# Optimization experiments

Hardware: AMD Instinct MI355X
Metric: run time of the kernel (lower is better)

Reference implementation:

```python
import jax, jax.numpy as jnp
import numpy as np

P = 7            # cfg.POOLING_SIZE (= group_size)
N_CLASSES = 21   # PASCAL VOC incl. background
SPATIAL_SCALE = 1.0 / 16.0


def _round_half_up(x):
    # matches C round() for non-negative roi coords (jnp.round is banker's)
    return jnp.floor(x + 0.5)


def psroi_pool(feat, rois, out_dim):
    """Position-sensitive RoI average pooling via integral images.
    feat: [B, out_dim*P*P, H, W]; rois: [N, 5] (batch_idx, x1, y1, x2, y2).
    Returns [N, out_dim, P, P]."""
    B, C, H, W = feat.shape
    # summed-area table, zero-padded: S[b,c,h,w] = sum feat[b,c,:h,:w]
    S = jnp.cumsum(jnp.cumsum(feat, axis=2), axis=3)
    S = jnp.pad(S, ((0, 0), (0, 0), (1, 0), (1, 0)))

    b = rois[:, 0].astype(jnp.int32)
    x1 = _round_half_up(rois[:, 1]) * SPATIAL_SCALE
    y1 = _round_half_up(rois[:, 2]) * SPATIAL_SCALE
    x2 = _round_half_up(rois[:, 3] + 1.0) * SPATIAL_SCALE
    y2 = _round_half_up(rois[:, 4] + 1.0) * SPATIAL_SCALE
    roi_w = jnp.maximum(x2 - x1, 0.1)
    roi_h = jnp.maximum(y2 - y1, 0.1)
    bin_w = roi_w / P
    bin_h = roi_h / P

    g = jnp.arange(P, dtype=feat.dtype)
    hs = jnp.clip(jnp.floor(g[None] * bin_h[:, None] + y1[:, None]), 0, H).astype(jnp.int32)        # [N,P]
    he = jnp.clip(jnp.ceil((g[None] + 1.0) * bin_h[:, None] + y1[:, None]), 0, H).astype(jnp.int32)
    ws = jnp.clip(jnp.floor(g[None] * bin_w[:, None] + x1[:, None]), 0, W).astype(jnp.int32)
    we = jnp.clip(jnp.ceil((g[None] + 1.0) * bin_w[:, None] + x1[:, None]), 0, W).astype(jnp.int32)

    # channel for (ctop, gh, gw) is (ctop*P + gh)*P + gw == arange(C) reshaped
    c = jnp.arange(C, dtype=jnp.int32).reshape(1, out_dim, P, P)
    bi = b[:, None, None, None]
    h0 = hs[:, None, :, None]; h1 = he[:, None, :, None]
    w0 = ws[:, None, None, :]; w1 = we[:, None, None, :]
    # box-sum from integral image -> [N, out_dim, P, P]
    ssum = S[bi, c, h1, w1] - S[bi, c, h0, w1] - S[bi, c, h1, w0] + S[bi, c, h0, w0]

    dh = jnp.maximum(he - hs, 0)[:, None, :, None]
    dw = jnp.maximum(we - ws, 0)[:, None, None, :]
    area = (dh * dw).astype(feat.dtype)
    return jnp.where(area > 0, ssum / jnp.maximum(area, 1.0), 0.0)


def setup_inputs() -> dict:
    key = jax.random.key(0)
    k1, k2, k3, k4, k5 = jax.random.split(key, 5)
    B, Cin, H, W = 4, 2048, 64, 64
    base_feat = jax.random.normal(k1, (B, Cin, H, W), jnp.float32)
    w_conv1 = 0.01 * jax.random.normal(k2, (1024, Cin), jnp.float32)
    w_cls = 0.01 * jax.random.normal(k3, (N_CLASSES * P * P, 1024), jnp.float32)
    w_bbox = 0.001 * jax.random.normal(k4, (4 * N_CLASSES * P * P, 1024), jnp.float32)
    # 300 ROIs per image in image coords (image size = 16*H = 1024)
    n_per = 300
    ka, kb = jax.random.split(k5)
    xy1 = jax.random.uniform(ka, (B * n_per, 2), jnp.float32, 0.0, 900.0)
    wh = jax.random.uniform(kb, (B * n_per, 2), jnp.float32, 16.0, 160.0)
    xy2 = jnp.minimum(xy1 + wh, 1023.0)
    bidx = jnp.repeat(jnp.arange(B, dtype=jnp.float32), n_per)[:, None]
    rois = jnp.concatenate([bidx, xy1[:, 0:1], xy1[:, 1:2], xy2[:, 0:1], xy2[:, 1:2]], axis=1)
    return {"base_feat": base_feat, "rois": rois, "w_conv1": w_conv1, "w_cls": w_cls, "w_bbox": w_bbox}


def reference(base_feat, rois, w_conv1, w_cls, w_bbox):
    B = base_feat.shape[0]
    n_per = rois.shape[0] // B
    # 1x1 conv (no bias) + relu
    x = jax.nn.relu(jnp.einsum('oi,bihw->bohw', w_conv1, base_feat))
    # cls branch: 1x1 conv -> PSRoIPool -> PxP avgpool -> softmax
    cls_feat = jnp.einsum('oi,bihw->bohw', w_cls, x)
    pooled_cls = psroi_pool(cls_feat, rois, N_CLASSES)        # [N, 21, P, P]
    cls_score = pooled_cls.mean(axis=(2, 3))                   # [N, 21]
    cls_prob = jax.nn.softmax(cls_score, axis=1)
    # bbox branch: 1x1 conv -> PSRoIPool -> PxP avgpool
    bbox_feat = jnp.einsum('oi,bihw->bohw', w_bbox, x)
    pooled_loc = psroi_pool(bbox_feat, rois, 4 * N_CLASSES)    # [N, 84, P, P]
    bbox_pred = pooled_loc.mean(axis=(2, 3))                    # [N, 84]
    return cls_prob.reshape(B, n_per, -1), bbox_pred.reshape(B, n_per, -1)
```

## Files before the change

### kernel.cpp

```cpp
#include <hip/hip_runtime.h>
#include <cstdint>


typedef __attribute__((ext_vector_type(8))) short short8;
typedef __attribute__((ext_vector_type(4))) short short4v;
typedef __attribute__((ext_vector_type(4))) float f32x4;

#define OFF_FEATT 0ull
#define OFF_W1    67108864ull
#define OFF_X     71303168ull
#define OFF_WC    104857600ull
#define OFF_DESC  117702656ull
#define OFF_SCORE 119709696ull
#define OFF_P     0ull

__device__ __forceinline__ unsigned short f2bf(float f) {
  unsigned u = __float_as_uint(f);
  u += 0x7fffu + ((u >> 16) & 1u);
  return (unsigned short)(u >> 16);
}
__device__ __forceinline__ float bf2f(unsigned short h) {
  return __uint_as_float(((unsigned)h) << 16);
}

__device__ __forceinline__ int swz6(int k6, int key) {
  return ((((k6 >> 3) & 7) ^ key) << 3) | (k6 & 7);
}

__device__ __forceinline__ void gload16(const void* g, void* l) {
  __builtin_amdgcn_global_load_lds((const __attribute__((address_space(1))) void*)g,
                                   (__attribute__((address_space(3))) void*)l, 16, 0, 0);
}

__global__ __launch_bounds__(256) void k_cvt_w1(const float* __restrict__ src,
                                                unsigned short* __restrict__ dst) {
  int t = blockIdx.x * 256 + threadIdx.x;
  long e = (long)t * 4;
  if (e >= 1024 * 2048) return;
  int o = (int)(e >> 11), k = (int)(e & 2047);
  float4 q = *(const float4*)(src + e);
  short4v s = {(short)f2bf(q.x), (short)f2bf(q.y), (short)f2bf(q.z), (short)f2bf(q.w)};
  int kp = (k & ~63) | swz6(k & 63, o & 7);
  *(short4v*)(dst + (size_t)o * 2048 + kp) = s;
}

__global__ __launch_bounds__(256) void k_cvt_wcomb(const float* __restrict__ wcls,
                                                   const float* __restrict__ wbbox,
                                                   unsigned short* __restrict__ dst) {
  int t = blockIdx.x * 256 + threadIdx.x;
  if (t >= 128 * 49 * 256) return;
  size_t e = (size_t)t * 4;
  int c = (int)(e / 50176);
  int rem = (int)(e - (size_t)c * 50176);
  int ij = rem >> 10, k = rem & 1023;
  float4 q = make_float4(0.f, 0.f, 0.f, 0.f);
  if (c < 21)       q = *(const float4*)(wcls + (size_t)(c * 49 + ij) * 1024 + k);
  else if (c < 105) q = *(const float4*)(wbbox + (size_t)((c - 21) * 49 + ij) * 1024 + k);
  short4v s = {(short)f2bf(q.x), (short)f2bf(q.y), (short)f2bf(q.z), (short)f2bf(q.w)};
  int kp = (k & ~63) | swz6(k & 63, c & 7);
  *(short4v*)(dst + ((size_t)(c * 49 + ij) * 1024 + kp)) = s;
}

__global__ __launch_bounds__(256) void k_tpose(const float* __restrict__ src,
                                               unsigned short* __restrict__ dst) {
  __shared__ float tile[64][65];
  int s0 = blockIdx.x * 64, c0 = blockIdx.y * 64, b = blockIdx.z;
  int tx = threadIdx.x & 63, ty = threadIdx.x >> 6;
  const float* sp = src + ((size_t)b * 2048 + c0) * 4096 + s0;
#pragma unroll
  for (int i = 0; i < 16; i++) {
    int cl = ty * 16 + i;
    tile[cl][tx] = sp[(size_t)cl * 4096 + tx];
  }
  __syncthreads();
  unsigned short* dp = dst + ((size_t)b * 4096 + s0) * 2048 + c0;
  int c4 = (threadIdx.x & 15) * 4;
  int sy = threadIdx.x >> 4;
#pragma unroll
  for (int i = 0; i < 4; i++) {
    int sl = i * 16 + sy;
    int key = sl & 7;
    short4v v = {(short)f2bf(tile[c4 + 0][sl]), (short)f2bf(tile[c4 + 1][sl]),
                 (short)f2bf(tile[c4 + 2][sl]), (short)f2bf(tile[c4 + 3][sl])};
    *(short4v*)(dp + (size_t)sl * 2048 + swz6(c4, key)) = v;
  }
}

__global__ __launch_bounds__(256) void k_gemm_conv1(const short* __restrict__ A,
                                                    const short* __restrict__ Bw,
                                                    unsigned short* __restrict__ X) {
  int mt = blockIdx.x, nt = blockIdx.y, b = blockIdx.z;
  __shared__ short As[128 * 64];
  __shared__ short Bs[128 * 64];
  int tid = threadIdx.x, lane = tid & 63, wave = tid >> 6;
  int wm = wave >> 1, wn = wave & 1;
  f32x4 acc[4][4];
#pragma unroll
  for (int i = 0; i < 4; i++)
#pragma unroll
    for (int j = 0; j < 4; j++) acc[i][j] = (f32x4){0.f, 0.f, 0.f, 0.f};

  const short* Ab = A + ((size_t)b * 4096 + (size_t)mt * 128) * 2048;
  const short* Bb = Bw + (size_t)nt * 128 * 2048;
  int lr = lane >> 3;
  int lc = (lane & 7) * 8;
  int key = lane & 7;

  for (int k0 = 0; k0 < 2048; k0 += 64) {
#pragma unroll
    for (int i = 0; i < 4; i++) {
      int row = i * 32 + wave * 8 + lr;
      gload16(Ab + (size_t)row * 2048 + k0 + lc, (char*)As + (i * 32 + wave * 8) * 128);
      gload16(Bb + (size_t)row * 2048 + k0 + lc, (char*)Bs + (i * 32 + wave * 8) * 128);
    }
    __syncthreads();
#pragma unroll
    for (int kt = 0; kt < 2; kt++) {
      int ko = (((kt << 2) | (lane >> 4)) ^ key) << 3;
      short8 af[4], bfr[4];
#pragma unroll
      for (int i = 0; i < 4; i++)
        af[i] = *(const short8*)(As + (wm * 64 + i * 16 + (lane & 15)) * 64 + ko);
#pragma unroll
      for (int j = 0; j < 4; j++)
        bfr[j] = *(const short8*)(Bs + (wn * 64 + j * 16 + (lane & 15)) * 64 + ko);
#pragma unroll
      for (int i = 0; i < 4; i++)
#pragma unroll
        for (int j = 0; j < 4; j++)
          acc[i][j] = __builtin_amdgcn_mfma_f32_16x16x32_bf16(af[i], bfr[j], acc[i][j], 0, 0, 0);
    }
    __syncthreads();
  }
  unsigned short* Xo = X + ((size_t)b * 4096 + (size_t)mt * 128) * 1024 + nt * 128;
#pragma unroll
  for (int i = 0; i < 4; i++)
#pragma unroll
    for (int j = 0; j < 4; j++) {
      int row = wm * 64 + i * 16 + (lane >> 4) * 4;
      int col = wn * 64 + j * 16 + (lane & 15);
#pragma unroll
      for (int r = 0; r < 4; r++)
        Xo[(size_t)(row + r) * 1024 + col] = f2bf(fmaxf(acc[i][j][r], 0.f));
    }
}

__global__ __launch_bounds__(256) void k_desc(const float* __restrict__ rois,
                                              int* __restrict__ desc) {
  int t = blockIdx.x * 256 + threadIdx.x;
  if (t >= 1280 * 49) return;
  int roi = t / 49, ij = t - roi * 49;
  int* d = desc + (size_t)t * 8;
  if (roi >= 1200) { d[0] = 0; d[1] = 0; d[2] = 0; d[3] = 0; d[4] = 0; ((float*)d)[5] = 0.f; return; }
  const float* r = rois + (size_t)roi * 5;
  int b = (int)r[0];
  float x1 = __fmul_rn(floorf(__fadd_rn(r[1], 0.5f)), 0.0625f);
  float y1 = __fmul_rn(floorf(__fadd_rn(r[2], 0.5f)), 0.0625f);
  float x2 = __fmul_rn(floorf(__fadd_rn(__fadd_rn(r[3], 1.0f), 0.5f)), 0.0625f);
  float y2 = __fmul_rn(floorf(__fadd_rn(__fadd_rn(r[4], 1.0f), 0.5f)), 0.0625f);
  float bw = __fdiv_rn(fmaxf(__fsub_rn(x2, x1), 0.1f), 7.0f);
  float bh = __fdiv_rn(fmaxf(__fsub_rn(y2, y1), 0.1f), 7.0f);
  int i = ij / 7, j = ij - (ij / 7) * 7;
  float fi = (float)i, fj = (float)j;
  int hs = (int)fminf(fmaxf(floorf(__fadd_rn(__fmul_rn(fi, bh), y1)), 0.f), 64.f);
  int he = (int)fminf(fmaxf(ceilf(__fadd_rn(__fmul_rn(__fadd_rn(fi, 1.f), bh), y1)), 0.f), 64.f);
  int wsx = (int)fminf(fmaxf(floorf(__fadd_rn(__fmul_rn(fj, bw), x1)), 0.f), 64.f);
  int we = (int)fminf(fmaxf(ceilf(__fadd_rn(__fmul_rn(__fadd_rn(fj, 1.f), bw), x1)), 0.f), 64.f);
  int dh = max(he - hs, 0), dw = max(we - wsx, 0);
  float inv = (dh * dw > 0) ? 1.0f / (float)(dh * dw) : 0.f;
  d[0] = b; d[1] = hs; d[2] = he; d[3] = wsx; d[4] = we;
  ((float*)d)[5] = inv;
}

__global__ __launch_bounds__(256) void k_fusedpool(const unsigned short* __restrict__ Xb,
                                                   const int* __restrict__ desc,
                                                   const unsigned short* __restrict__ Wc,
                                                   unsigned short* __restrict__ P,
                                                   int nroi) {
  int mt = blockIdx.x;
  int ij = blockIdx.y;
  __shared__ short As[64 * 64];
  __shared__ short Bs[128 * 64];
  __shared__ int dsc[64][4];
  int tid = threadIdx.x, lane = tid & 63, wave = tid >> 6;

  if (tid < 64) {
    const int* d = desc + ((size_t)(mt * 64 + tid) * 49 + ij) * 8;
    int b = d[0], hs = d[1], he = d[2], wsx = d[3], we = d[4];
    dsc[tid][0] = (b * 64 + hs) * 64 + wsx;
    dsc[tid][1] = max(he - hs, 0);
    dsc[tid][2] = max(we - wsx, 0);
    dsc[tid][3] = d[5];
  }
  __syncthreads();

  f32x4 acc[4][2];
#pragma unroll
  for (int i = 0; i < 4; i++)
#pragma unroll
    for (int j = 0; j < 2; j++) acc[i][j] = (f32x4){0.f, 0.f, 0.f, 0.f};

  const unsigned short* Bb = Wc + (size_t)ij * 1024;
  int lr = lane >> 3, lc = (lane & 7) * 8;
  int key = lane & 7;
  int r8 = tid >> 3;
  int k8 = tid & 7;

  for (int k0 = 0; k0 < 1024; k0 += 64) {
#pragma unroll
    for (int i = 0; i < 4; i++) {
      int row = i * 32 + wave * 8 + lr;
      gload16(Bb + (size_t)row * (49 * 1024) + k0 + lc, (char*)Bs + (i * 32 + wave * 8) * 128);
    }
#pragma unroll
    for (int p = 0; p < 2; p++) {
      int r = p * 32 + r8;
      int cs = dsc[r][0], dh = dsc[r][1], dw = dsc[r][2];
      float inv = __int_as_float(dsc[r][3]);
      float a0 = 0.f, a1 = 0.f, a2 = 0.f, a3 = 0.f, a4 = 0.f, a5 = 0.f, a6 = 0.f, a7 = 0.f;
      const unsigned short* xp = Xb + (size_t)cs * 1024 + k0 + k8 * 8;
      for (int h = 0; h < dh; h++) {
        const unsigned short* xq = xp;
        for (int w = 0; w < dw; w++) {
          short8 v = *(const short8*)xq;
          a0 += bf2f((unsigned short)v[0]); a1 += bf2f((unsigned short)v[1]);
          a2 += bf2f((unsigned short)v[2]); a3 += bf2f((unsigned short)v[3]);
          a4 += bf2f((unsigned short)v[4]); a5 += bf2f((unsigned short)v[5]);
          a6 += bf2f((unsigned short)v[6]); a7 += bf2f((unsigned short)v[7]);
          xq += 1024;
        }
        xp += 64 * 1024;
      }
      short8 o = {(short)f2bf(a0 * inv), (short)f2bf(a1 * inv),
                  (short)f2bf(a2 * inv), (short)f2bf(a3 * inv),
                  (short)f2bf(a4 * inv), (short)f2bf(a5 * inv),
                  (short)f2bf(a6 * inv), (short)f2bf(a7 * inv)};
      *(short8*)(As + r * 64 + ((k8 ^ (r & 7)) << 3)) = o;
    }
    __syncthreads();
#pragma unroll
    for (int kt = 0; kt < 2; kt++) {
      int ko = (((kt << 2) | (lane >> 4)) ^ key) << 3;
      short8 af[4], bfr[2];
#pragma unroll
      for (int i = 0; i < 4; i++)
        af[i] = *(const short8*)(As + (i * 16 + (lane & 15)) * 64 + ko);
#pragma unroll
      for (int j = 0; j < 2; j++)
        bfr[j] = *(const short8*)(Bs + (wave * 32 + j * 16 + (lane & 15)) * 64 + ko);
#pragma unroll
      for (int i = 0; i < 4; i++)
#pragma unroll
        for (int j = 0; j < 2; j++)
          acc[i][j] = __builtin_amdgcn_mfma_f32_16x16x32_bf16(af[i], bfr[j], acc[i][j], 0, 0, 0);
    }
    __syncthreads();
  }
  unsigned short* Pb = P + (size_t)ij * nroi * 112;
#pragma unroll
  for (int i = 0; i < 4; i++)
#pragma unroll
    for (int j = 0; j < 2; j++) {
      int cc = wave * 32 + j * 16 + (lane & 15);
      if (cc < 112) {
        int rbase = mt * 64 + i * 16 + (lane >> 4) * 4;
#pragma unroll
        for (int r = 0; r < 4; r++)
          Pb[(size_t)(rbase + r) * 112 + cc] = f2bf(acc[i][j][r]);
      }
    }
}

__global__ __launch_bounds__(256) void k_reduce(const unsigned short* __restrict__ P,
                                                float* __restrict__ score, int nroi) {
  int t = blockIdx.x * 256 + threadIdx.x;
  if (t >= nroi * 112) return;
  int roi = t / 112, c = t - roi * 112;
  float s = 0.f;
#pragma unroll 7
  for (int ij = 0; ij < 49; ij++) s += bf2f(P[(size_t)ij * nroi * 112 + t]);
  score[(size_t)roi * 128 + c] = s;
}

__global__ __launch_bounds__(256) void k_final(const float* __restrict__ score,
                                               float* __restrict__ out) {
  int t = blockIdx.x * 256 + threadIdx.x;
  if (t < 1200) {
    float s[21];
    float mx = -1e30f;
#pragma unroll
    for (int c = 0; c < 21; c++) {
      s[c] = score[(size_t)t * 128 + c] * (1.f / 49.f);
      mx = fmaxf(mx, s[c]);
    }
    float sum = 0.f;
#pragma unroll
    for (int c = 0; c < 21; c++) { s[c] = expf(s[c] - mx); sum += s[c]; }
    float rs = 1.f / sum;
#pragma unroll
    for (int c = 0; c < 21; c++) out[(size_t)t * 21 + c] = s[c] * rs;
  }
  if (t < 100800) {
    int roi = t / 84, c = t - (t / 84) * 84;
    out[25200 + t] = score[(size_t)roi * 128 + 21 + c] * (1.f / 49.f);
  }
}

extern "C" void kernel_launch(void* const* d_in, const int* in_sizes, int n_in,
                              void* d_out, int out_size, void* d_ws, size_t ws_size,
                              hipStream_t stream) {
  const float* base_feat = (const float*)d_in[0];
  const float* rois      = (const float*)d_in[1];
  const float* w_conv1   = (const float*)d_in[2];
  const float* w_cls     = (const float*)d_in[3];
  const float* w_bbox    = (const float*)d_in[4];
  float* out = (float*)d_out;
  char* ws = (char*)d_ws;

  unsigned short* featT = (unsigned short*)(ws + OFF_FEATT);
  unsigned short* w1b   = (unsigned short*)(ws + OFF_W1);
  unsigned short* X     = (unsigned short*)(ws + OFF_X);
  unsigned short* Wc    = (unsigned short*)(ws + OFF_WC);
  int*            desc  = (int*)(ws + OFF_DESC);
  float*          score = (float*)(ws + OFF_SCORE);
  unsigned short* P     = (unsigned short*)(ws + OFF_P);

  k_cvt_w1<<<2048, 256, 0, stream>>>(w_conv1, w1b);
  k_cvt_wcomb<<<6272, 256, 0, stream>>>(w_cls, w_bbox, Wc);
  k_tpose<<<dim3(64, 32, 4), 256, 0, stream>>>(base_feat, featT);
  k_gemm_conv1<<<dim3(32, 8, 4), 256, 0, stream>>>((const short*)featT, (const short*)w1b, X);
  k_desc<<<245, 256, 0, stream>>>(rois, desc);
  k_fusedpool<<<dim3(20, 49), 256, 0, stream>>>(X, desc, Wc, P, 1280);
  k_reduce<<<560, 256, 0, stream>>>(P, score, 1280);
  k_final<<<394, 256, 0, stream>>>(score, out);
}
```

Baseline: 428.0 us.

## Split-K the fused pooling GEMM and merge prep kernels into one launch

The weight-conversion, RoI-descriptor and feature-transpose kernels are merged into one launch, with block-index ranges picking the role. The fused pool+GEMM kernel now splits its 1024-wide K dimension into two halves over a new grid z dimension. That doubles the block count to improve CU occupancy and tail balance. Each half writes its own partial buffer, and the reduce kernel sums 98 partials instead of 49, which adds extra partial-buffer traffic.

After: 413.1 us. 3.5% less time.

```diff
diff --git a/kernel.cpp b/kernel.cpp
--- a/kernel.cpp
+++ b/kernel.cpp
@@ -32,57 +32,85 @@
                                    (__attribute__((address_space(3))) void*)l, 16, 0, 0);
 }
 
-__global__ __launch_bounds__(256) void k_cvt_w1(const float* __restrict__ src,
-                                                unsigned short* __restrict__ dst) {
-  int t = blockIdx.x * 256 + threadIdx.x;
-  long e = (long)t * 4;
-  if (e >= 1024 * 2048) return;
-  int o = (int)(e >> 11), k = (int)(e & 2047);
-  float4 q = *(const float4*)(src + e);
-  short4v s = {(short)f2bf(q.x), (short)f2bf(q.y), (short)f2bf(q.z), (short)f2bf(q.w)};
-  int kp = (k & ~63) | swz6(k & 63, o & 7);
-  *(short4v*)(dst + (size_t)o * 2048 + kp) = s;
-}
-
-__global__ __launch_bounds__(256) void k_cvt_wcomb(const float* __restrict__ wcls,
-                                                   const float* __restrict__ wbbox,
-                                                   unsigned short* __restrict__ dst) {
-  int t = blockIdx.x * 256 + threadIdx.x;
-  if (t >= 128 * 49 * 256) return;
-  size_t e = (size_t)t * 4;
-  int c = (int)(e / 50176);
-  int rem = (int)(e - (size_t)c * 50176);
-  int ij = rem >> 10, k = rem & 1023;
-  float4 q = make_float4(0.f, 0.f, 0.f, 0.f);
-  if (c < 21)       q = *(const float4*)(wcls + (size_t)(c * 49 + ij) * 1024 + k);
-  else if (c < 105) q = *(const float4*)(wbbox + (size_t)((c - 21) * 49 + ij) * 1024 + k);
-  short4v s = {(short)f2bf(q.x), (short)f2bf(q.y), (short)f2bf(q.z), (short)f2bf(q.w)};
-  int kp = (k & ~63) | swz6(k & 63, c & 7);
-  *(short4v*)(dst + ((size_t)(c * 49 + ij) * 1024 + kp)) = s;
-}
-
-__global__ __launch_bounds__(256) void k_tpose(const float* __restrict__ src,
-                                               unsigned short* __restrict__ dst) {
+__global__ __launch_bounds__(256) void k_prep(const float* __restrict__ w_conv1,
+                                              const float* __restrict__ wcls,
+                                              const float* __restrict__ wbbox,
+                                              const float* __restrict__ rois,
+                                              const float* __restrict__ base_feat,
+                                              unsigned short* __restrict__ w1b,
+                                              unsigned short* __restrict__ Wc,
+                                              int* __restrict__ desc,
+                                              unsigned short* __restrict__ featT) {
   __shared__ float tile[64][65];
-  int s0 = blockIdx.x * 64, c0 = blockIdx.y * 64, b = blockIdx.z;
-  int tx = threadIdx.x & 63, ty = threadIdx.x >> 6;
-  const float* sp = src + ((size_t)b * 2048 + c0) * 4096 + s0;
-#pragma unroll
-  for (int i = 0; i < 16; i++) {
-    int cl = ty * 16 + i;
-    tile[cl][tx] = sp[(size_t)cl * 4096 + tx];
-  }
-  __syncthreads();
-  unsigned short* dp = dst + ((size_t)b * 4096 + s0) * 2048 + c0;
-  int c4 = (threadIdx.x & 15) * 4;
-  int sy = threadIdx.x >> 4;
-#pragma unroll
-  for (int i = 0; i < 4; i++) {
-    int sl = i * 16 + sy;
-    int key = sl & 7;
-    short4v v = {(short)f2bf(tile[c4 + 0][sl]), (short)f2bf(tile[c4 + 1][sl]),
-                 (short)f2bf(tile[c4 + 2][sl]), (short)f2bf(tile[c4 + 3][sl])};
-    *(short4v*)(dp + (size_t)sl * 2048 + swz6(c4, key)) = v;
+  int bid = blockIdx.x;
+  if (bid < 2048) {
+    int t = bid * 256 + threadIdx.x;
+    long e = (long)t * 4;
+    int o = (int)(e >> 11), k = (int)(e & 2047);
+    float4 q = *(const float4*)(w_conv1 + e);
+    short4v s = {(short)f2bf(q.x), (short)f2bf(q.y), (short)f2bf(q.z), (short)f2bf(q.w)};
+    int kp = (k & ~63) | swz6(k & 63, o & 7);
+    *(short4v*)(w1b + (size_t)o * 2048 + kp) = s;
+  } else if (bid < 8320) {
+    int t = (bid - 2048) * 256 + threadIdx.x;
+    size_t e = (size_t)t * 4;
+    int c = (int)(e / 50176);
+    int rem = (int)(e - (size_t)c * 50176);
+    int ij = rem >> 10, k = rem & 1023;
+    float4 q = make_float4(0.f, 0.f, 0.f, 0.f);
+    if (c < 21)       q = *(const float4*)(wcls + (size_t)(c * 49 + ij) * 1024 + k);
+    else if (c < 105) q = *(const float4*)(wbbox + (size_t)((c - 21) * 49 + ij) * 1024 + k);
+    short4v s = {(short)f2bf(q.x), (short)f2bf(q.y), (short)f2bf(q.z), (short)f2bf(q.w)};
+    int kp = (k & ~63) | swz6(k & 63, c & 7);
+    *(short4v*)(Wc + ((size_t)(c * 49 + ij) * 1024 + kp)) = s;
+  } else if (bid < 8565) {
+    int t = (bid - 8320) * 256 + threadIdx.x;
+    if (t >= 1280 * 49) return;
+    int roi = t / 49, ij = t - roi * 49;
+    int* d = desc + (size_t)t * 8;
+    if (roi >= 1200) { d[0] = 0; d[1] = 0; d[2] = 0; d[3] = 0; d[4] = 0; ((float*)d)[5] = 0.f; return; }
+    const float* r = rois + (size_t)roi * 5;
+    int b = (int)r[0];
+    float x1 = __fmul_rn(floorf(__fadd_rn(r[1], 0.5f)), 0.0625f);
+    float y1 = __fmul_rn(floorf(__fadd_rn(r[2], 0.5f)), 0.0625f);
+    float x2 = __fmul_rn(floorf(__fadd_rn(__fadd_rn(r[3], 1.0f), 0.5f)), 0.0625f);
+    float y2 = __fmul_rn(floorf(__fadd_rn(__fadd_rn(r[4], 1.0f), 0.5f)), 0.0625f);
+    float bw = __fdiv_rn(fmaxf(__fsub_rn(x2, x1), 0.1f), 7.0f);
+    float bh = __fdiv_rn(fmaxf(__fsub_rn(y2, y1), 0.1f), 7.0f);
+    int i = ij / 7, j = ij - (ij / 7) * 7;
+    float fi = (float)i, fj = (float)j;
+    int hs = (int)fminf(fmaxf(floorf(__fadd_rn(__fmul_rn(fi, bh), y1)), 0.f), 64.f);
+    int he = (int)fminf(fmaxf(ceilf(__fadd_rn(__fmul_rn(__fadd_rn(fi, 1.f), bh), y1)), 0.f), 64.f);
+    int wsx = (int)fminf(fmaxf(floorf(__fadd_rn(__fmul_rn(fj, bw), x1)), 0.f), 64.f);
+    int we = (int)fminf(fmaxf(ceilf(__fadd_rn(__fmul_rn(__fadd_rn(fj, 1.f), bw), x1)), 0.f), 64.f);
+    int dh = max(he - hs, 0), dw = max(we - wsx, 0);
+    float inv = (dh * dw > 0) ? 1.0f / (float)(dh * dw) : 0.f;
+    d[0] = b; d[1] = hs; d[2] = he; d[3] = wsx; d[4] = we;
+    ((float*)d)[5] = inv;
+  } else {
+    int t = bid - 8565;
+    int s0 = (t & 63) * 64;
+    int c0 = ((t >> 6) & 31) * 64;
+    int b = t >> 11;
+    int tx = threadIdx.x & 63, ty = threadIdx.x >> 6;
+    const float* sp = base_feat + ((size_t)b * 2048 + c0) * 4096 + s0;
+#pragma unroll
+    for (int i = 0; i < 16; i++) {
+      int cl = ty * 16 + i;
+      tile[cl][tx] = sp[(size_t)cl * 4096 + tx];
+    }
+    __syncthreads();
+    unsigned short* dp = featT + ((size_t)b * 4096 + s0) * 2048 + c0;
+    int c4 = (threadIdx.x & 15) * 4;
+    int sy = threadIdx.x >> 4;
+#pragma unroll
+    for (int i = 0; i < 4; i++) {
+      int sl = i * 16 + sy;
+      int key = sl & 7;
+      short4v v = {(short)f2bf(tile[c4 + 0][sl]), (short)f2bf(tile[c4 + 1][sl]),
+                   (short)f2bf(tile[c4 + 2][sl]), (short)f2bf(tile[c4 + 3][sl])};
+      *(short4v*)(dp + (size_t)sl * 2048 + swz6(c4, key)) = v;
+    }
   }
 }
 
@@ -145,33 +173,6 @@
     }
 }
 
-__global__ __launch_bounds__(256) void k_desc(const float* __restrict__ rois,
-                                              int* __restrict__ desc) {
-  int t = blockIdx.x * 256 + threadIdx.x;
-  if (t >= 1280 * 49) return;
-  int roi = t / 49, ij = t - roi * 49;
-  int* d = desc + (size_t)t * 8;
-  if (roi >= 1200) { d[0] = 0; d[1] = 0; d[2] = 0; d[3] = 0; d[4] = 0; ((float*)d)[5] = 0.f; return; }
-  const float* r = rois + (size_t)roi * 5;
-  int b = (int)r[0];
-  float x1 = __fmul_rn(floorf(__fadd_rn(r[1], 0.5f)), 0.0625f);
-  float y1 = __fmul_rn(floorf(__fadd_rn(r[2], 0.5f)), 0.0625f);
-  float x2 = __fmul_rn(floorf(__fadd_rn(__fadd_rn(r[3], 1.0f), 0.5f)), 0.0625f);
-  float y2 = __fmul_rn(floorf(__fadd_rn(__fadd_rn(r[4], 1.0f), 0.5f)), 0.0625f);
-  float bw = __fdiv_rn(fmaxf(__fsub_rn(x2, x1), 0.1f), 7.0f);
-  float bh = __fdiv_rn(fmaxf(__fsub_rn(y2, y1), 0.1f), 7.0f);
-  int i = ij / 7, j = ij - (ij / 7) * 7;
-  float fi = (float)i, fj = (float)j;
-  int hs = (int)fminf(fmaxf(floorf(__fadd_rn(__fmul_rn(fi, bh), y1)), 0.f), 64.f);
-  int he = (int)fminf(fmaxf(ceilf(__fadd_rn(__fmul_rn(__fadd_rn(fi, 1.f), bh), y1)), 0.f), 64.f);
-  int wsx = (int)fminf(fmaxf(floorf(__fadd_rn(__fmul_rn(fj, bw), x1)), 0.f), 64.f);
-  int we = (int)fminf(fmaxf(ceilf(__fadd_rn(__fmul_rn(__fadd_rn(fj, 1.f), bw), x1)), 0.f), 64.f);
-  int dh = max(he - hs, 0), dw = max(we - wsx, 0);
-  float inv = (dh * dw > 0) ? 1.0f / (float)(dh * dw) : 0.f;
-  d[0] = b; d[1] = hs; d[2] = he; d[3] = wsx; d[4] = we;
-  ((float*)d)[5] = inv;
-}
-
 __global__ __launch_bounds__(256) void k_fusedpool(const unsigned short* __restrict__ Xb,
                                                    const int* __restrict__ desc,
                                                    const unsigned short* __restrict__ Wc,
@@ -179,6 +180,7 @@
                                                    int nroi) {
   int mt = blockIdx.x;
   int ij = blockIdx.y;
+  int kh = blockIdx.z;
   __shared__ short As[64 * 64];
   __shared__ short Bs[128 * 64];
   __shared__ int dsc[64][4];
@@ -206,7 +208,8 @@
   int r8 = tid >> 3;
   int k8 = tid & 7;
 
-  for (int k0 = 0; k0 < 1024; k0 += 64) {
+  int kbeg = kh * 512, kend = kbeg + 512;
+  for (int k0 = kbeg; k0 < kend; k0 += 64) {
 #pragma unroll
     for (int i = 0; i < 4; i++) {
       int row = i * 32 + wave * 8 + lr;
@@ -256,7 +259,7 @@
     }
     __syncthreads();
   }
-  unsigned short* Pb = P + (size_t)ij * nroi * 112;
+  unsigned short* Pb = P + (size_t)(kh * 49 + ij) * nroi * 112;
 #pragma unroll
   for (int i = 0; i < 4; i++)
 #pragma unroll
@@ -278,7 +281,7 @@
   int roi = t / 112, c = t - roi * 112;
   float s = 0.f;
 #pragma unroll 7
-  for (int ij = 0; ij < 49; ij++) s += bf2f(P[(size_t)ij * nroi * 112 + t]);
+  for (int ij = 0; ij < 98; ij++) s += bf2f(P[(size_t)ij * nroi * 112 + t]);
   score[(size_t)roi * 128 + c] = s;
 }
 
@@ -325,12 +328,10 @@
   float*          score = (float*)(ws + OFF_SCORE);
   unsigned short* P     = (unsigned short*)(ws + OFF_P);
 
-  k_cvt_w1<<<2048, 256, 0, stream>>>(w_conv1, w1b);
-  k_cvt_wcomb<<<6272, 256, 0, stream>>>(w_cls, w_bbox, Wc);
-  k_tpose<<<dim3(64, 32, 4), 256, 0, stream>>>(base_feat, featT);
+  k_prep<<<16757, 256, 0, stream>>>(w_conv1, w_cls, w_bbox, rois, base_feat,
+                                    w1b, Wc, desc, featT);
   k_gemm_conv1<<<dim3(32, 8, 4), 256, 0, stream>>>((const short*)featT, (const short*)w1b, X);
-  k_desc<<<245, 256, 0, stream>>>(rois, desc);
-  k_fusedpool<<<dim3(20, 49), 256, 0, stream>>>(X, desc, Wc, P, 1280);
+  k_fusedpool<<<dim3(20, 49, 2), 256, 0, stream>>>(X, desc, Wc, P, 1280);
   k_reduce<<<560, 256, 0, stream>>>(P, score, 1280);
   k_final<<<394, 256, 0, stream>>>(score, out);
 }
```
